# Optimization experiments

Measured on AMD Instinct MI355X. Metric: run time of the kernel, lower is better.

## Reference

```python
import jax, jax.numpy as jnp
import numpy as np

KERNEL = 5
DILATION = 2
PAD = DILATION * (KERNEL - 1) // 2  # symmetric 'same' padding along the conv axis


def _conv(x, w, b, padding, rhs_dilation):
    y = jax.lax.conv_general_dilated(
        x, w, window_strides=(1, 1), padding=padding,
        rhs_dilation=rhs_dilation,
        dimension_numbers=("NCHW", "OIHW", "NCHW"))
    return y + b[None, :, None, None]


def h_transform(x):
    # shear: [B,C,H,W] -> [B,C,H,2W-1], row i shifted right by i
    B, C, H, W = x.shape
    x = jnp.pad(x, ((0, 0), (0, 0), (0, 0), (0, W)))
    x = x.reshape(B, C, -1)[..., :-W]
    return x.reshape(B, C, H, 2 * W - 1)


def inv_h_transform(x):
    # inverse shear, assumes input [B,C,H,2H-1] -> [B,C,H,H]
    B, C, H, _ = x.shape
    x = x.reshape(B, C, -1)
    x = jnp.pad(x, ((0, 0), (0, 0), (0, H)))
    return x.reshape(B, C, H, 2 * H)[..., :H]


def v_transform(x):
    return jnp.transpose(h_transform(jnp.transpose(x, (0, 1, 3, 2))), (0, 1, 3, 2))


def inv_v_transform(x):
    return jnp.transpose(inv_h_transform(jnp.transpose(x, (0, 1, 3, 2))), (0, 1, 3, 2))


def setup_inputs() -> dict:
    key = jax.random.key(0)
    ks = jax.random.split(key, 9)
    B, C, H, W = 8, 256, 128, 128
    outc = C // 4
    x = jax.random.normal(ks[0], (B, C, H, W), dtype=jnp.float32)
    w_h = jax.random.normal(ks[1], (outc, C, 1, KERNEL), dtype=jnp.float32) * 0.02
    b_h = jax.random.normal(ks[2], (outc,), dtype=jnp.float32) * 0.02
    w_v = jax.random.normal(ks[3], (outc, C, KERNEL, 1), dtype=jnp.float32) * 0.02
    b_v = jax.random.normal(ks[4], (outc,), dtype=jnp.float32) * 0.02
    w_d1 = jax.random.normal(ks[5], (outc, C, KERNEL, 1), dtype=jnp.float32) * 0.02
    b_d1 = jax.random.normal(ks[6], (outc,), dtype=jnp.float32) * 0.02
    w_d2 = jax.random.normal(ks[7], (outc, C, 1, KERNEL), dtype=jnp.float32) * 0.02
    b_d2 = jax.random.normal(ks[8], (outc,), dtype=jnp.float32) * 0.02
    return {"x": x, "w_h": w_h, "b_h": b_h, "w_v": w_v, "b_v": b_v,
            "w_d1": w_d1, "b_d1": b_d1, "w_d2": w_d2, "b_d2": b_d2}


def reference(x, w_h, b_h, w_v, b_v, w_d1, b_d1, w_d2, b_d2):
    # branch 1: horizontal dilated conv (1,k)
    x1 = _conv(x, w_h, b_h, padding=((0, 0), (PAD, PAD)), rhs_dilation=(1, DILATION))
    # branch 2: vertical dilated conv (k,1)
    x2 = _conv(x, w_v, b_v, padding=((PAD, PAD), (0, 0)), rhs_dilation=(DILATION, 1))
    # branch 3: diagonal via h-shear + vertical conv + inverse shear
    x3 = inv_h_transform(_conv(h_transform(x), w_d1, b_d1,
                                padding=((PAD, PAD), (0, 0)), rhs_dilation=(DILATION, 1)))
    # branch 4: anti-diagonal via v-shear + horizontal conv + inverse shear
    x4 = inv_v_transform(_conv(v_transform(x), w_d2, b_d2,
                                padding=((0, 0), (PAD, PAD)), rhs_dilation=(1, DILATION)))
    return jnp.concatenate([x1, x2, x3, x4], axis=1)
```

## Files before the change

kernel.cpp:

```cpp
#include <hip/hip_runtime.h>
#include <hip/hip_bf16.h>


typedef __attribute__((ext_vector_type(8))) __bf16 bf16x8;
typedef __attribute__((ext_vector_type(4))) float f32x4;

#define HH 128
#define WW 128
#define CIN 256
#define NCHUNK 8
#define CHUNK 32
#define COLS 136
#define TROWS 6
#define BUF_SHORTS (TROWS*COLS*CHUNK)
#define WPG (40*64*32)

__device__ __forceinline__ ushort f2bf(float f) {
    union { float f; unsigned u; } v; v.f = f;
    unsigned r = v.u + 0x7FFF + ((v.u >> 16) & 1);
    return (ushort)(r >> 16);
}

__global__ void repack_w(const float* __restrict__ w0, const float* __restrict__ w1,
                         const float* __restrict__ w2, const float* __restrict__ w3,
                         ushort* __restrict__ wp) {
    int idx = blockIdx.x * 256 + threadIdx.x;
    int g   = idx / WPG;
    int rem = idx - g * WPG;
    int s   = rem >> 11;
    int r2  = rem & 2047;
    int m   = r2 >> 5;
    int kk  = r2 & 31;
    int k   = s % 5;
    int cg  = s / 5;
    const float* w = (g == 0) ? w0 : (g == 1) ? w1 : (g == 2) ? w2 : w3;
    wp[idx] = f2bf(w[(m * CIN + cg * 32 + kk) * 5 + k]);
}

__global__ __launch_bounds__(512, 2)
void asterisk_mfma7(const float* __restrict__ x,
                    const ushort* __restrict__ wp,
                    const float* __restrict__ b0, const float* __restrict__ b1,
                    const float* __restrict__ b2, const float* __restrict__ b3,
                    float* __restrict__ out) {
    __shared__ __align__(16) short xs[BUF_SHORTS];

    const int t    = threadIdx.x;
    const int lane = t & 63;
    const int wid  = t >> 6;
    const int g    = wid & 3;
    const int l    = wid >> 2;
    const int m16  = lane & 15;
    const int h    = lane >> 4;

    const int id = blockIdx.x;
    const int b  = id & 7;
    const int p  = id >> 3;
    const int i0 = 4 * (p >> 1) + (p & 1);
    const int i  = i0 + 2 * l;

    for (int e = t; e < TROWS * 8 * CHUNK; e += 512) {
        int r  = e >> 8;
        int pc = (e >> 5) & 7;
        int c  = e & 31;
        int col = (pc < 4) ? pc : 128 + pc;
        xs[(r * COLS + col) * CHUNK + c] = 0;
    }

    const float* bias = (g == 0) ? b0 : (g == 1) ? b1 : (g == 2) ? b2 : b3;
    f32x4 acc[4][8];
#pragma unroll
    for (int mb = 0; mb < 4; ++mb) {
        f32x4 bv;
#pragma unroll
        for (int rr = 0; rr < 4; ++rr) bv[rr] = bias[mb * 16 + h * 4 + rr];
#pragma unroll
        for (int nb = 0; nb < 8; ++nb) acc[mb][nb] = bv;
    }

    const int rh = t >> 8;
    const int cg = (t >> 5) & 7;
    const int q  = t & 31;
    const float* xb = x + (size_t)b * CIN * HH * WW;

    bool rowok[3];
    const float* rowp[3];
#pragma unroll
    for (int r2 = 0; r2 < 3; ++r2) {
        int r   = rh * 3 + r2;
        int row = i0 + 2 * r - 4;
        rowok[r2] = (unsigned)row < HH;
        rowp[r2]  = xb + (size_t)(cg * 4) * (HH * WW) + (size_t)(rowok[r2] ? row : 0) * WW + q * 4;
    }

    float4 st[3][4];

    auto loadchunk = [&](int cc) {
        size_t coff = (size_t)cc * CHUNK * (HH * WW);
#pragma unroll
        for (int r2 = 0; r2 < 3; ++r2) {
            if (rowok[r2]) {
                const float* src = rowp[r2] + coff;
                st[r2][0] = *(const float4*)(src);
                st[r2][1] = *(const float4*)(src + HH * WW);
                st[r2][2] = *(const float4*)(src + 2 * (HH * WW));
                st[r2][3] = *(const float4*)(src + 3 * (HH * WW));
            } else {
                float4 z = {0.f, 0.f, 0.f, 0.f};
                st[r2][0] = z; st[r2][1] = z; st[r2][2] = z; st[r2][3] = z;
            }
        }
    };

    auto writechunk = [&]() {
        int slot = cg >> 1;
        int sub  = (cg & 1) * 4;
#pragma unroll
        for (int r2 = 0; r2 < 3; ++r2) {
            int r = rh * 3 + r2;
#pragma unroll
            for (int jj = 0; jj < 4; ++jj) {
                int col = q * 4 + 4 + jj;
                int sl  = slot ^ ((col >> 2) & 3);
                float f0 = ((const float*)&st[r2][0])[jj];
                float f1 = ((const float*)&st[r2][1])[jj];
                float f2 = ((const float*)&st[r2][2])[jj];
                float f3 = ((const float*)&st[r2][3])[jj];
                __hip_bfloat162 lo = __float22bfloat162_rn(make_float2(f0, f1));
                __hip_bfloat162 hi = __float22bfloat162_rn(make_float2(f2, f3));
                uint2 pk;
                pk.x = *(unsigned*)&lo;
                pk.y = *(unsigned*)&hi;
                int wi = (r * COLS + col) * CHUNK + sl * 8 + sub;
                wi ^= ((col >> 4) & 1) << 5;
                *(uint2*)&xs[wi] = pk;
            }
        }
    };

    const ushort* wl = wp + (size_t)g * WPG + m16 * 32 + h * 8;
    bf16x8 a_cur[4], a_nxt[4];
#pragma unroll
    for (int mb = 0; mb < 4; ++mb)
        a_cur[mb] = *(const bf16x8*)(wl + mb * 512);

    loadchunk(0);

    for (int cc = 0; cc < NCHUNK; ++cc) {
        __syncthreads();
        writechunk();
        __syncthreads();
        if (cc < NCHUNK - 1) loadchunk(cc + 1);

#pragma unroll
        for (int k = 0; k < 5; ++k) {
            int s = cc * 5 + k;
            if (s < 39) {
                const ushort* wk1 = wl + (size_t)(s + 1) * 2048;
#pragma unroll
                for (int mb = 0; mb < 4; ++mb)
                    a_nxt[mb] = *(const bf16x8*)(wk1 + mb * 512);
            }
            int rbase = (g == 0) ? 2 : (g == 3 ? 4 - k : k);
            int r  = rbase + l;
            int dj = (g == 1) ? 0 : (g == 2 ? 4 - 2 * k : 2 * k - 4);
            int col0 = m16 + dj + 4;
            int sl   = h ^ ((col0 >> 2) & 3);
            int base = (r * COLS + col0) * CHUNK + sl * 8;
            base ^= ((col0 >> 4) & 1) << 5;

            __builtin_amdgcn_s_setprio(1);
#pragma unroll
            for (int nb = 0; nb < 8; ++nb) {
                int idx = (base + nb * 16 * CHUNK) ^ ((nb & 1) << 5);
                bf16x8 bf = *(const bf16x8*)(&xs[idx]);
#pragma unroll
                for (int mb = 0; mb < 4; ++mb)
                    acc[mb][nb] = __builtin_amdgcn_mfma_f32_16x16x32_bf16(
                        a_cur[mb], bf, acc[mb][nb], 0, 0, 0);
            }
            __builtin_amdgcn_s_setprio(0);
            if (s < 39) {
#pragma unroll
                for (int mb = 0; mb < 4; ++mb) a_cur[mb] = a_nxt[mb];
            }
        }
    }

    size_t obase = (((size_t)b * 256 + g * 64) * HH + i) * WW;
#pragma unroll
    for (int mb = 0; mb < 4; ++mb)
#pragma unroll
        for (int rr = 0; rr < 4; ++rr) {
            float* op = out + obase + (size_t)(mb * 16 + h * 4 + rr) * HH * WW + m16;
#pragma unroll
            for (int nb = 0; nb < 8; ++nb)
                op[nb * 16] = acc[mb][nb][rr];
        }
}

extern "C" void kernel_launch(void* const* d_in, const int* in_sizes, int n_in,
                              void* d_out, int out_size, void* d_ws, size_t ws_size,
                              hipStream_t stream) {
    const float* x    = (const float*)d_in[0];
    const float* w_h  = (const float*)d_in[1];
    const float* b_h  = (const float*)d_in[2];
    const float* w_v  = (const float*)d_in[3];
    const float* b_v  = (const float*)d_in[4];
    const float* w_d1 = (const float*)d_in[5];
    const float* b_d1 = (const float*)d_in[6];
    const float* w_d2 = (const float*)d_in[7];
    const float* b_d2 = (const float*)d_in[8];
    float* out = (float*)d_out;
    ushort* wpack = (ushort*)d_ws;

    repack_w<<<1280, 256, 0, stream>>>(w_h, w_v, w_d1, w_d2, wpack);
    asterisk_mfma7<<<512, 512, 0, stream>>>(x, wpack, b_h, b_v, b_d1, b_d2, out);
}
```

Before: 106.1 us.

## Double-buffer LDS input chunks and software-pipeline B-fragment loads

```diff
diff --git a/kernel.cpp b/kernel.cpp
--- a/kernel.cpp
+++ b/kernel.cpp
@@ -38,12 +38,12 @@
 }
 
 __global__ __launch_bounds__(512, 2)
-void asterisk_mfma7(const float* __restrict__ x,
+void asterisk_mfma8(const float* __restrict__ x,
                     const ushort* __restrict__ wp,
                     const float* __restrict__ b0, const float* __restrict__ b1,
                     const float* __restrict__ b2, const float* __restrict__ b3,
                     float* __restrict__ out) {
-    __shared__ __align__(16) short xs[BUF_SHORTS];
+    __shared__ __align__(16) short xs[2][BUF_SHORTS];
 
     const int t    = threadIdx.x;
     const int lane = t & 63;
@@ -59,12 +59,15 @@
     const int i0 = 4 * (p >> 1) + (p & 1);
     const int i  = i0 + 2 * l;
 
-    for (int e = t; e < TROWS * 8 * CHUNK; e += 512) {
-        int r  = e >> 8;
-        int pc = (e >> 5) & 7;
-        int c  = e & 31;
+    for (int e = t; e < 2 * TROWS * 8 * CHUNK; e += 512) {
+        int s    = e;
+        int bufi = s >= TROWS * 8 * CHUNK;
+        if (bufi) s -= TROWS * 8 * CHUNK;
+        int r  = s >> 8;
+        int pc = (s >> 5) & 7;
+        int c  = s & 31;
         int col = (pc < 4) ? pc : 128 + pc;
-        xs[(r * COLS + col) * CHUNK + c] = 0;
+        xs[bufi][(r * COLS + col) * CHUNK + c] = 0;
     }
 
     const float* bias = (g == 0) ? b0 : (g == 1) ? b1 : (g == 2) ? b2 : b3;
@@ -90,7 +93,8 @@
         int r   = rh * 3 + r2;
         int row = i0 + 2 * r - 4;
         rowok[r2] = (unsigned)row < HH;
-        rowp[r2]  = xb + (size_t)(cg * 4) * (HH * WW) + (size_t)(rowok[r2] ? row : 0) * WW + q * 4;
+        rowp[r2]  = xb + (size_t)(cg * 4) * (HH * WW)
+                       + (size_t)(rowok[r2] ? row : 0) * WW + q * 4;
     }
 
     float4 st[3][4];
@@ -112,7 +116,7 @@
         }
     };
 
-    auto writechunk = [&]() {
+    auto writechunk = [&](int sel) {
         int slot = cg >> 1;
         int sub  = (cg & 1) * 4;
 #pragma unroll
@@ -133,34 +137,30 @@
                 pk.y = *(unsigned*)&hi;
                 int wi = (r * COLS + col) * CHUNK + sl * 8 + sub;
                 wi ^= ((col >> 4) & 1) << 5;
-                *(uint2*)&xs[wi] = pk;
+                *(uint2*)&xs[sel][wi] = pk;
             }
         }
     };
 
     const ushort* wl = wp + (size_t)g * WPG + m16 * 32 + h * 8;
-    bf16x8 a_cur[4], a_nxt[4];
-#pragma unroll
-    for (int mb = 0; mb < 4; ++mb)
-        a_cur[mb] = *(const bf16x8*)(wl + mb * 512);
 
     loadchunk(0);
+    writechunk(0);
+    __syncthreads();
+    loadchunk(1);
 
     for (int cc = 0; cc < NCHUNK; ++cc) {
-        __syncthreads();
-        writechunk();
-        __syncthreads();
-        if (cc < NCHUNK - 1) loadchunk(cc + 1);
+        const int sel = cc & 1;
+        const short* xsel = xs[sel];
 
 #pragma unroll
         for (int k = 0; k < 5; ++k) {
-            int s = cc * 5 + k;
-            if (s < 39) {
-                const ushort* wk1 = wl + (size_t)(s + 1) * 2048;
-#pragma unroll
-                for (int mb = 0; mb < 4; ++mb)
-                    a_nxt[mb] = *(const bf16x8*)(wk1 + mb * 512);
-            }
+            const ushort* wk = wl + (size_t)(cc * 5 + k) * 2048;
+            bf16x8 a[4];
+#pragma unroll
+            for (int mb = 0; mb < 4; ++mb)
+                a[mb] = *(const bf16x8*)(wk + mb * 512);
+
             int rbase = (g == 0) ? 2 : (g == 3 ? 4 - k : k);
             int r  = rbase + l;
             int dj = (g == 1) ? 0 : (g == 2 ? 4 - 2 * k : 2 * k - 4);
@@ -169,21 +169,28 @@
             int base = (r * COLS + col0) * CHUNK + sl * 8;
             base ^= ((col0 >> 4) & 1) << 5;
 
+            bf16x8 bfc = *(const bf16x8*)(&xsel[base]);
             __builtin_amdgcn_s_setprio(1);
 #pragma unroll
             for (int nb = 0; nb < 8; ++nb) {
-                int idx = (base + nb * 16 * CHUNK) ^ ((nb & 1) << 5);
-                bf16x8 bf = *(const bf16x8*)(&xs[idx]);
+                bf16x8 bfn;
+                if (nb < 7) {
+                    int idx = (base + (nb + 1) * 16 * CHUNK) ^ (((nb + 1) & 1) << 5);
+                    bfn = *(const bf16x8*)(&xsel[idx]);
+                }
 #pragma unroll
                 for (int mb = 0; mb < 4; ++mb)
                     acc[mb][nb] = __builtin_amdgcn_mfma_f32_16x16x32_bf16(
-                        a_cur[mb], bf, acc[mb][nb], 0, 0, 0);
+                        a[mb], bfc, acc[mb][nb], 0, 0, 0);
+                if (nb < 7) bfc = bfn;
             }
             __builtin_amdgcn_s_setprio(0);
-            if (s < 39) {
-#pragma unroll
-                for (int mb = 0; mb < 4; ++mb) a_cur[mb] = a_nxt[mb];
-            }
+        }
+
+        if (cc < NCHUNK - 1) {
+            writechunk(sel ^ 1);
+            if (cc < NCHUNK - 2) loadchunk(cc + 2);
+            __syncthreads();
         }
     }
 
@@ -215,5 +222,5 @@
     ushort* wpack = (ushort*)d_ws;
 
     repack_w<<<1280, 256, 0, stream>>>(w_h, w_v, w_d1, w_d2, wpack);
-    asterisk_mfma7<<<512, 512, 0, stream>>>(x, wpack, b_h, b_v, b_d1, b_d2, out);
-}
+    asterisk_mfma8<<<512, 512, 0, stream>>>(x, wpack, b_h, b_v, b_d1, b_d2, out);
+}
```

After: 100.9 us. -4.9%, faster.
